# Kernel tuning notes

Hardware: AMD Instinct MI355X
Metric: run time of the kernel (lower is better)

The kernel has to match this reference:

```python
import jax, jax.numpy as jnp
import numpy as np
from jax import lax

B = 1024          # batch
R = 100           # number of radical heads (TOP_RADICALS)


def _conv(x, w, b, padding):
    y = lax.conv_general_dilated(
        x, w, window_strides=(1, 1), padding=padding,
        dimension_numbers=('NCHW', 'OIHW', 'NCHW'))
    return y + b[None, :, None, None]


def _maxpool2(x):
    return lax.reduce_window(x, -jnp.inf, lax.max,
                             (1, 1, 2, 2), (1, 1, 2, 2), 'VALID')


def setup_inputs() -> dict:
    key = jax.random.key(0)
    ks = jax.random.split(key, 20)
    s = 0.05
    inp = {
        'x': jax.random.normal(ks[0], (B, 1, 98, 98), jnp.float32),
        'conv1_w': jax.random.normal(ks[1], (6, 1, 3, 3), jnp.float32) * s,
        'conv1_b': jnp.zeros((6,), jnp.float32),
        'conv2_w': jax.random.normal(ks[2], (4, 6, 6, 6), jnp.float32) * s,
        'conv2_b': jnp.zeros((4,), jnp.float32),
        'conv3_w': jax.random.normal(ks[3], (2, 4, 3, 3), jnp.float32) * s,
        'conv3_b': jnp.zeros((2,), jnp.float32),
        'fc1_w': jax.random.normal(ks[4], (200, 400), jnp.float32) * s,
        'fc1_b': jnp.zeros((400,), jnp.float32),
        'fc2_w': jax.random.normal(ks[5], (400, 200), jnp.float32) * s,
        'fc2_b': jnp.zeros((200,), jnp.float32),
        # all R per-radical heads stacked: Linear(200,140)->(140,84)->(84,42)->(42,4)
        'h1_w': jax.random.normal(ks[6], (R, 200, 140), jnp.float32) * s,
        'h1_b': jnp.zeros((R, 140), jnp.float32),
        'h2_w': jax.random.normal(ks[7], (R, 140, 84), jnp.float32) * s,
        'h2_b': jnp.zeros((R, 84), jnp.float32),
        'h3_w': jax.random.normal(ks[8], (R, 84, 42), jnp.float32) * s,
        'h3_b': jnp.zeros((R, 42), jnp.float32),
        'h4_w': jax.random.normal(ks[9], (R, 42, 4), jnp.float32) * s,
        'h4_b': jnp.zeros((R, 4), jnp.float32),
    }
    return inp


def reference(x, conv1_w, conv1_b, conv2_w, conv2_b, conv3_w, conv3_b,
              fc1_w, fc1_b, fc2_w, fc2_b,
              h1_w, h1_b, h2_w, h2_b, h3_w, h3_b, h4_w, h4_b):
    # conv trunk: conv -> relu -> maxpool, x3
    x = _maxpool2(jax.nn.relu(_conv(x, conv1_w, conv1_b, [(1, 1), (1, 1)])))  # [B,6,49,49]
    x = _maxpool2(jax.nn.relu(_conv(x, conv2_w, conv2_b, 'VALID')))           # [B,4,22,22]
    x = _maxpool2(jax.nn.relu(_conv(x, conv3_w, conv3_b, 'VALID')))           # [B,2,10,10]
    x = x.reshape(x.shape[0], -1)                                             # [B,200]
    # shared MLP trunk
    x = jax.nn.relu(x @ fc1_w + fc1_b)   # [B,400]
    x = jax.nn.relu(x @ fc2_w + fc2_b)   # [B,200]
    # R independent 4-layer heads, fused into batched einsums
    h = jax.nn.relu(jnp.einsum('bd,rdh->brh', x, h1_w) + h1_b)  # [B,R,140]
    h = jax.nn.relu(jnp.einsum('brd,rdh->brh', h, h2_w) + h2_b)  # [B,R,84]
    h = jax.nn.relu(jnp.einsum('brd,rdh->brh', h, h3_w) + h3_b)  # [B,R,42]
    h = jnp.einsum('brd,rdh->brh', h, h4_w) + h4_b               # [B,R,4]
    # torch.cat over heads along dim=1 == reshape [B, R*4]
    return h.reshape(h.shape[0], -1)
```

## Files before the change

### kernel.cpp

```cpp
#include <hip/hip_runtime.h>

#define NB 1024
#define NR 100

typedef _Float16 half_t;
typedef half_t f16x8 __attribute__((ext_vector_type(8)));
typedef float f32x4 __attribute__((ext_vector_type(4)));

__device__ __forceinline__ int kmap2(int g, int j) {
    return g*4 + (j & 3) + ((j >> 2) << 4);
}

#define GLDS(gsrc, ldst) \
    __builtin_amdgcn_global_load_lds( \
        (const __attribute__((address_space(1))) void*)(gsrc), \
        (__attribute__((address_space(3))) void*)(ldst), 16, 0, 0)

__global__ __launch_bounds__(256) void conv1_k(const float* __restrict__ x,
        const float* __restrict__ w, const float* __restrict__ bias,
        float* __restrict__ out) {
    __shared__ float img[98*98];
    __shared__ float ws[54];
    __shared__ float bs[6];
    const int b = blockIdx.x;
    const int tid = threadIdx.x;
    const float* xb = x + (size_t)b * 9604;
    for (int i = tid; i < 2401; i += 256)
        ((float4*)img)[i] = ((const float4*)xb)[i];
    if (tid < 54) ws[tid] = w[tid];
    if (tid < 6) bs[tid] = bias[tid];
    __syncthreads();
    for (int pos = tid; pos < 2401; pos += 256) {
        const int py = pos / 49, px = pos % 49;
        const int y0 = 2*py - 1, x0 = 2*px - 1;
        float p[4][4];
        #pragma unroll
        for (int dy = 0; dy < 4; ++dy) {
            const int iy = y0 + dy;
            #pragma unroll
            for (int dx = 0; dx < 4; ++dx) {
                const int ix = x0 + dx;
                p[dy][dx] = (iy >= 0 && iy < 98 && ix >= 0 && ix < 98)
                            ? img[iy*98 + ix] : 0.f;
            }
        }
        #pragma unroll
        for (int c = 0; c < 6; ++c) {
            float v0 = bs[c], v1 = bs[c], v2 = bs[c], v3 = bs[c];
            #pragma unroll
            for (int ky = 0; ky < 3; ++ky) {
                #pragma unroll
                for (int kx = 0; kx < 3; ++kx) {
                    const float wv = ws[c*9 + ky*3 + kx];
                    v0 = fmaf(wv, p[ky  ][kx  ], v0);
                    v1 = fmaf(wv, p[ky  ][kx+1], v1);
                    v2 = fmaf(wv, p[ky+1][kx  ], v2);
                    v3 = fmaf(wv, p[ky+1][kx+1], v3);
                }
            }
            float m = fmaxf(fmaxf(v0, v1), fmaxf(v2, v3));
            out[((size_t)b*6 + c)*2401 + pos] = fmaxf(m, 0.f);
        }
    }
}

__global__ __launch_bounds__(256, 4) void conv2_k(const float* __restrict__ in,
        const float* __restrict__ w, const float* __restrict__ bias,
        float* __restrict__ out) {
    __shared__ float smc[6*27*28];
    __shared__ float ws[864];
    __shared__ float bs[4];
    const int blk = blockIdx.x;
    const int b  = blk >> 2;
    const int qy = (blk >> 1) & 1, qx = blk & 1;
    const int r0 = qy*22, c0 = qx*22;
    const int tid = threadIdx.x;
    const float* src = in + (size_t)b * 14406;
    for (int idx = tid; idx < 6*27*27; idx += 256) {
        const int ic  = idx / 729;
        const int rem = idx - ic*729;
        const int rr  = rem / 27;
        const int cc  = rem - rr*27;
        smc[ic*756 + rr*28 + cc] = src[ic*2401 + (r0+rr)*49 + c0 + cc];
    }
    for (int i = tid; i < 864; i += 256) ws[i] = w[i];
    if (tid < 4) bs[tid] = bias[tid];
    __syncthreads();
    if (tid < 242) {
        const int ocg = tid / 121;
        const int p   = tid - ocg*121;
        const int py  = p / 11, px = p - py*11;
        const int y0  = 2*py, x0 = 2*px;
        float acc[2][4];
        #pragma unroll
        for (int o = 0; o < 2; ++o) {
            const float bv = bs[ocg*2 + o];
            acc[o][0] = acc[o][1] = acc[o][2] = acc[o][3] = bv;
        }
        #pragma unroll
        for (int ic = 0; ic < 6; ++ic) {
            float pt[7][7];
            const float* basep = smc + ic*756 + y0*28 + x0;
            #pragma unroll
            for (int u = 0; u < 7; ++u) {
                const float* rb = basep + u*28;
                *(float2*)&pt[u][0] = *(const float2*)&rb[0];
                *(float2*)&pt[u][2] = *(const float2*)&rb[2];
                *(float2*)&pt[u][4] = *(const float2*)&rb[4];
                pt[u][6] = rb[6];
            }
            #pragma unroll
            for (int o = 0; o < 2; ++o) {
                const float* wp = ws + ((ocg*2 + o)*6 + ic)*36;
                #pragma unroll
                for (int ky = 0; ky < 6; ++ky) {
                    #pragma unroll
                    for (int kx = 0; kx < 6; ++kx) {
                        const float wv = wp[ky*6 + kx];
                        acc[o][0] = fmaf(wv, pt[ky  ][kx  ], acc[o][0]);
                        acc[o][1] = fmaf(wv, pt[ky  ][kx+1], acc[o][1]);
                        acc[o][2] = fmaf(wv, pt[ky+1][kx  ], acc[o][2]);
                        acc[o][3] = fmaf(wv, pt[ky+1][kx+1], acc[o][3]);
                    }
                }
            }
        }
        const int PY = qy*11 + py, PX = qx*11 + px;
        #pragma unroll
        for (int o = 0; o < 2; ++o) {
            const int oc = ocg*2 + o;
            float m = fmaxf(fmaxf(acc[o][0], acc[o][1]),
                            fmaxf(acc[o][2], acc[o][3]));
            out[(((size_t)b*4 + oc)*22 + PY)*22 + PX] = fmaxf(m, 0.f);
        }
    }
}

__global__ __launch_bounds__(256) void conv3_k(const float* __restrict__ in,
        const float* __restrict__ w, const float* __restrict__ bias,
        float* __restrict__ out) {
    __shared__ float sm[1936];
    __shared__ float ws[72];
    __shared__ float bs[2];
    const int b = blockIdx.x;
    const int tid = threadIdx.x;
    const float* src = in + (size_t)b * 1936;
    for (int i = tid; i < 484; i += 256)
        ((float4*)sm)[i] = ((const float4*)src)[i];
    if (tid < 72) ws[tid] = w[tid];
    if (tid < 2) bs[tid] = bias[tid];
    __syncthreads();
    if (tid < 200) {
        const int c = tid / 100;
        const int rem = tid % 100;
        const int py = rem / 10, px = rem % 10;
        const int y0 = 2*py, x0 = 2*px;
        float a0, a1, a2, a3;
        a0 = a1 = a2 = a3 = bs[c];
        #pragma unroll
        for (int ic = 0; ic < 4; ++ic) {
            float p[4][4];
            const float* base = sm + ic*484 + y0*22 + x0;
            #pragma unroll
            for (int u = 0; u < 4; ++u)
                #pragma unroll
                for (int v = 0; v < 4; ++v)
                    p[u][v] = base[u*22 + v];
            const float* wp = ws + (c*4 + ic)*9;
            #pragma unroll
            for (int ky = 0; ky < 3; ++ky) {
                #pragma unroll
                for (int kx = 0; kx < 3; ++kx) {
                    const float wv = wp[ky*3 + kx];
                    a0 = fmaf(wv, p[ky  ][kx  ], a0);
                    a1 = fmaf(wv, p[ky  ][kx+1], a1);
                    a2 = fmaf(wv, p[ky+1][kx  ], a2);
                    a3 = fmaf(wv, p[ky+1][kx+1], a3);
                }
            }
        }
        float m = fmaxf(fmaxf(a0, a1), fmaxf(a2, a3));
        out[(size_t)b*200 + tid] = fmaxf(m, 0.f);
    }
}

template<bool G0OUT>
__global__ __launch_bounds__(256, 4) void gemm_k(
        const float* __restrict__ A, int lda,
        const float* __restrict__ W, const float* __restrict__ bias,
        float* __restrict__ C, int ldc,
        int M, int N, int K,
        half_t* __restrict__ g0h, half_t* __restrict__ g0l) {
    __shared__ float As[32][132];
    __shared__ float Ws[32][64];
    const int m0 = blockIdx.y * 128;
    const int n0 = blockIdx.x * 64;
    const int tid = threadIdx.x;
    const int ti = tid >> 4, tj = tid & 15;
    float acc[8][4];
    #pragma unroll
    for (int i = 0; i < 8; ++i)
        #pragma unroll
        for (int j = 0; j < 4; ++j) acc[i][j] = 0.f;

    for (int k0 = 0; k0 < K; k0 += 32) {
        #pragma unroll
        for (int i = 0; i < 4; ++i) {
            const int f = tid + i*256;
            const int m = f >> 3, kg = f & 7;
            const int kk = kg*4;
            float4 v = make_float4(0.f, 0.f, 0.f, 0.f);
            if (k0 + kk < K)
                v = *(const float4*)(A + (long)(m0 + m)*lda + k0 + kk);
            As[kk+0][m] = v.x;
            As[kk+1][m] = v.y;
            As[kk+2][m] = v.z;
            As[kk+3][m] = v.w;
        }
        #pragma unroll
        for (int i = 0; i < 2; ++i) {
            const int f = tid + i*256;
            const int kk = f >> 4, cg = f & 15;
            const int n = n0 + cg*4;
            float4 v = make_float4(0.f, 0.f, 0.f, 0.f);
            if (k0 + kk < K) {
                const float* wp = W + (long)(k0 + kk)*N;
                if (n + 3 < N) v = *(const float4*)(wp + n);
                else {
                    if (n+0 < N) v.x = wp[n+0];
                    if (n+1 < N) v.y = wp[n+1];
                    if (n+2 < N) v.z = wp[n+2];
                }
            }
            *(float4*)&Ws[kk][cg*4] = v;
        }
        __syncthreads();
        #pragma unroll
        for (int kk = 0; kk < 32; ++kk) {
            float a[8], wv[4];
            *(float4*)&a[0] = *(const float4*)&As[kk][ti*8];
            *(float4*)&a[4] = *(const float4*)&As[kk][ti*8 + 4];
            *(float4*)&wv[0] = *(const float4*)&Ws[kk][tj*4];
            #pragma unroll
            for (int i = 0; i < 8; ++i)
                #pragma unroll
                for (int j = 0; j < 4; ++j)
                    acc[i][j] = fmaf(a[i], wv[j], acc[i][j]);
        }
        __syncthreads();
    }

    const int nb = n0 + tj*4;
    float bv[4] = {0.f, 0.f, 0.f, 0.f};
    #pragma unroll
    for (int e = 0; e < 4; ++e) if (nb + e < N) bv[e] = bias[nb + e];

    if (!G0OUT) {
        #pragma unroll
        for (int i = 0; i < 8; ++i) {
            const long m = m0 + ti*8 + i;
            if (nb + 3 < N) {
                float4 v;
                v.x = fmaxf(acc[i][0] + bv[0], 0.f);
                v.y = fmaxf(acc[i][1] + bv[1], 0.f);
                v.z = fmaxf(acc[i][2] + bv[2], 0.f);
                v.w = fmaxf(acc[i][3] + bv[3], 0.f);
                *(float4*)(C + m*(long)ldc + nb) = v;
            } else {
                #pragma unroll
                for (int j = 0; j < 4; ++j)
                    if (nb + j < N)
                        C[m*(long)ldc + nb + j] = fmaxf(acc[i][j] + bv[j], 0.f);
            }
        }
    } else {
        #pragma unroll
        for (int i = 0; i < 8; ++i) {
            const int m = m0 + ti*8 + i;
            #pragma unroll
            for (int j = 0; j < 4; ++j) {
                const int k = nb + j;
                if (k < N) {
                    const float v = fmaxf(acc[i][j] + bv[j], 0.f);
                    const half_t hi = (half_t)v;
                    const half_t lo = (half_t)(v - (float)hi);
                    const int kc = k >> 5, klo = k & 31;
                    const int h = klo >> 4, rm = klo & 15;
                    const int gg = rm >> 2, rr = rm & 3;
                    const size_t idx =
                        ((size_t)((m >> 4)*7 + kc)*64 + (gg << 4) + (m & 15))*8
                        + h*4 + rr;
                    g0h[idx] = hi;
                    g0l[idx] = lo;
                }
            }
        }
    }
}

__global__ __launch_bounds__(256) void wsplit_k(
        const float* __restrict__ w1, const float* __restrict__ w2,
        const float* __restrict__ w3, const float* __restrict__ w4,
        half_t* __restrict__ f1h, half_t* __restrict__ f1l,
        half_t* __restrict__ f2h, half_t* __restrict__ f2l,
        half_t* __restrict__ f3h, half_t* __restrict__ f3l,
        half_t* __restrict__ f4h, half_t* __restrict__ f4l) {
    __shared__ float lds[32*140];
    const int cx = blockIdx.x, r = blockIdx.y, tid = threadIdx.x;
    int K, N, KC, NF, kc;
    const float* src;
    half_t *dh, *dl;
    if (cx < 7)       { K=200; N=140; KC=7; NF=9; kc=cx;    src=w1; dh=f1h; dl=f1l; }
    else if (cx < 12) { K=140; N=84;  KC=5; NF=6; kc=cx-7;  src=w2; dh=f2h; dl=f2l; }
    else if (cx < 15) { K=84;  N=42;  KC=3; NF=3; kc=cx-12; src=w3; dh=f3h; dl=f3l; }
    else              { K=42;  N=4;   KC=2; NF=1; kc=cx-15; src=w4; dh=f4h; dl=f4l; }
    const float* sb = src + (size_t)r * K * N;
    for (int i = tid; i < 32*N; i += 256) {
        const int kk = i / N, n = i - kk*N;
        const int kg = kc*32 + kk;
        lds[kk*N + n] = (kg < K) ? sb[(size_t)kg*N + n] : 0.f;
    }
    __syncthreads();
    const size_t base = ((size_t)r*KC + kc)*NF*512;
    for (int e = tid; e < NF*512; e += 256) {
        const int nf = e >> 9, rem = e & 511;
        const int l = rem >> 3, j = rem & 7;
        const int g = l >> 4, c = l & 15;
        const int kl = kmap2(g, j);
        const int n = nf*16 + c;
        const float v = (n < N) ? lds[kl*N + n] : 0.f;
        const half_t hi = (half_t)v;
        const half_t lo = (half_t)(v - (float)hi);
        dh[base + (size_t)nf*512 + rem] = hi;
        dl[base + (size_t)nf*512 + rem] = lo;
    }
}

#define MFMA(a, b, c) __builtin_amdgcn_mfma_f32_16x16x32_f16(a, b, c, 0, 0, 0)

__global__ __launch_bounds__(256, 4) void head_k(
        const half_t* __restrict__ g0h, const half_t* __restrict__ g0l,
        const half_t* __restrict__ w1h, const half_t* __restrict__ w1l,
        const half_t* __restrict__ w2h, const half_t* __restrict__ w2l,
        const half_t* __restrict__ w3h, const half_t* __restrict__ w3l,
        const half_t* __restrict__ w4h, const half_t* __restrict__ w4l,
        const float* __restrict__ b1, const float* __restrict__ b2,
        const float* __restrict__ b3, const float* __restrict__ b4,
        float* __restrict__ out) {
    __shared__ half_t wb[18*512];
    __shared__ float bl[270];
    const int bid = blockIdx.x;
    const int cx  = bid & 7;
    const int kb  = bid >> 3;
    const int r   = ((kb >> 3) << 3) + cx;
    if (r >= NR) return;
    const int mt  = kb & 7;
    const int tid = threadIdx.x;
    if (tid < 140) bl[tid]       = b1[(size_t)r*140 + tid];
    if (tid < 84)  bl[140 + tid] = b2[(size_t)r*84  + tid];
    if (tid < 42)  bl[224 + tid] = b3[(size_t)r*42  + tid];
    if (tid < 4)   bl[266 + tid] = b4[(size_t)r*4   + tid];
    const int w = tid >> 6, l = tid & 63;
    const int g4 = ((l >> 4) & 3) * 4;
    const int mb0 = mt*8 + w*2;
    const size_t loff = (size_t)l * 8;

    f32x4 a1[2][9] = {};
    for (int kc = 0; kc < 7; ++kc) {
        const half_t* hs = w1h + ((size_t)r*7 + kc)*9*512;
        const half_t* ls = w1l + ((size_t)r*7 + kc)*9*512;
        #pragma unroll
        for (int p0 = 0; p0 < 3; ++p0) {
            const int p = w + p0*4;
            if (p < 9) {
                GLDS(hs + (size_t)p*512 + loff, wb + p*512);
                GLDS(ls + (size_t)p*512 + loff, wb + (9+p)*512);
            }
        }
        f16x8 bh[2], blo[2];
        #pragma unroll
        for (int mb = 0; mb < 2; ++mb) {
            const size_t bo = ((size_t)(mb0 + mb)*7 + kc)*512 + loff;
            bh[mb]  = *(const f16x8*)(g0h + bo);
            blo[mb] = *(const f16x8*)(g0l + bo);
        }
        __syncthreads();
        #pragma unroll
        for (int nf = 0; nf < 9; ++nf) {
            const f16x8 wh = *(const f16x8*)(wb + nf*512 + loff);
            const f16x8 wl = *(const f16x8*)(wb + (9+nf)*512 + loff);
            #pragma unroll
            for (int mb = 0; mb < 2; ++mb) {
                a1[mb][nf] = MFMA(wh, bh[mb],  a1[mb][nf]);
                a1[mb][nf] = MFMA(wh, blo[mb], a1[mb][nf]);
                a1[mb][nf] = MFMA(wl, bh[mb],  a1[mb][nf]);
            }
        }
        __syncthreads();
    }
    f16x8 b2h[2][5], b2l[2][5];
    #pragma unroll
    for (int kc = 0; kc < 5; ++kc)
        #pragma unroll
        for (int h = 0; h < 2; ++h) {
            const int nf = kc*2 + h;
            #pragma unroll
            for (int mb = 0; mb < 2; ++mb)
                #pragma unroll
                for (int rr = 0; rr < 4; ++rr) {
                    float v = 0.f;
                    if (nf < 9) {
                        const int n = nf*16 + g4 + rr;
                        v = (n < 140) ? fmaxf(a1[mb][nf][rr] + bl[n], 0.f) : 0.f;
                    }
                    const half_t hi = (half_t)v;
                    const half_t lo = (half_t)(v - (float)hi);
                    b2h[mb][kc][h*4+rr] = hi;
                    b2l[mb][kc][h*4+rr] = lo;
                }
        }
    f32x4 a2[2][6] = {};
    for (int kc = 0; kc < 5; ++kc) {
        const half_t* hs = w2h + ((size_t)r*5 + kc)*6*512;
        const half_t* ls = w2l + ((size_t)r*5 + kc)*6*512;
        #pragma unroll
        for (int p0 = 0; p0 < 2; ++p0) {
            const int p = w + p0*4;
            if (p < 6) {
                GLDS(hs + (size_t)p*512 + loff, wb + p*512);
                GLDS(ls + (size_t)p*512 + loff, wb + (6+p)*512);
            }
        }
        __syncthreads();
        #pragma unroll
        for (int nf = 0; nf < 6; ++nf) {
            const f16x8 wh = *(const f16x8*)(wb + nf*512 + loff);
            const f16x8 wl = *(const f16x8*)(wb + (6+nf)*512 + loff);
            #pragma unroll
            for (int mb = 0; mb < 2; ++mb) {
                a2[mb][nf] = MFMA(wh, b2h[mb][kc], a2[mb][nf]);
                a2[mb][nf] = MFMA(wh, b2l[mb][kc], a2[mb][nf]);
                a2[mb][nf] = MFMA(wl, b2h[mb][kc], a2[mb][nf]);
            }
        }
        __syncthreads();
    }
    f16x8 b3h[2][3], b3l[2][3];
    #pragma unroll
    for (int kc = 0; kc < 3; ++kc)
        #pragma unroll
        for (int h = 0; h < 2; ++h) {
            const int nf = kc*2 + h;
            #pragma unroll
            for (int mb = 0; mb < 2; ++mb)
                #pragma unroll
                for (int rr = 0; rr < 4; ++rr) {
                    float v = 0.f;
                    if (nf < 6) {
                        const int n = nf*16 + g4 + rr;
                        v = (n < 84) ? fmaxf(a2[mb][nf][rr] + bl[140 + n], 0.f) : 0.f;
                    }
                    const half_t hi = (half_t)v;
                    const half_t lo = (half_t)(v - (float)hi);
                    b3h[mb][kc][h*4+rr] = hi;
                    b3l[mb][kc][h*4+rr] = lo;
                }
        }
    f32x4 a3[2][3] = {};
    for (int kc = 0; kc < 3; ++kc) {
        const half_t* hs = w3h + ((size_t)r*3 + kc)*3*512;
        const half_t* ls = w3l + ((size_t)r*3 + kc)*3*512;
        {
            const int p = w;
            if (p < 3) {
                GLDS(hs + (size_t)p*512 + loff, wb + p*512);
                GLDS(ls + (size_t)p*512 + loff, wb + (3+p)*512);
            }
        }
        __syncthreads();
        #pragma unroll
        for (int nf = 0; nf < 3; ++nf) {
            const f16x8 wh = *(const f16x8*)(wb + nf*512 + loff);
            const f16x8 wl = *(const f16x8*)(wb + (3+nf)*512 + loff);
            #pragma unroll
            for (int mb = 0; mb < 2; ++mb) {
                a3[mb][nf] = MFMA(wh, b3h[mb][kc], a3[mb][nf]);
                a3[mb][nf] = MFMA(wh, b3l[mb][kc], a3[mb][nf]);
                a3[mb][nf] = MFMA(wl, b3h[mb][kc], a3[mb][nf]);
            }
        }
        __syncthreads();
    }
    f16x8 b4h[2][2], b4l[2][2];
    #pragma unroll
    for (int kc = 0; kc < 2; ++kc)
        #pragma unroll
        for (int h = 0; h < 2; ++h) {
            const int nf = kc*2 + h;
            #pragma unroll
            for (int mb = 0; mb < 2; ++mb)
                #pragma unroll
                for (int rr = 0; rr < 4; ++rr) {
                    float v = 0.f;
                    if (nf < 3) {
                        const int n = nf*16 + g4 + rr;
                        v = (n < 42) ? fmaxf(a3[mb][nf][rr] + bl[224 + n], 0.f) : 0.f;
                    }
                    const half_t hi = (half_t)v;
                    const half_t lo = (half_t)(v - (float)hi);
                    b4h[mb][kc][h*4+rr] = hi;
                    b4l[mb][kc][h*4+rr] = lo;
                }
        }
    f32x4 a4[2] = {};
    #pragma unroll
    for (int kc = 0; kc < 2; ++kc) {
        const size_t wo = ((size_t)r*2 + kc)*512 + loff;
        const f16x8 wh = *(const f16x8*)(w4h + wo);
        const f16x8 wl = *(const f16x8*)(w4l + wo);
        #pragma unroll
        for (int mb = 0; mb < 2; ++mb) {
            a4[mb] = MFMA(wh, b4h[mb][kc], a4[mb]);
            a4[mb] = MFMA(wh, b4l[mb][kc], a4[mb]);
            a4[mb] = MFMA(wl, b4h[mb][kc], a4[mb]);
        }
    }
    if ((l >> 4) == 0) {
        #pragma unroll
        for (int mb = 0; mb < 2; ++mb) {
            const int b = (mb0 + mb)*16 + (l & 15);
            float4 o;
            o.x = a4[mb][0] + bl[266];
            o.y = a4[mb][1] + bl[267];
            o.z = a4[mb][2] + bl[268];
            o.w = a4[mb][3] + bl[269];
            *(float4*)(out + (size_t)b*400 + r*4) = o;
        }
    }
}

extern "C" void kernel_launch(void* const* d_in, const int* in_sizes, int n_in,
                              void* d_out, int out_size, void* d_ws, size_t ws_size,
                              hipStream_t stream) {
    const float* x    = (const float*)d_in[0];
    const float* c1w  = (const float*)d_in[1];
    const float* c1b  = (const float*)d_in[2];
    const float* c2w  = (const float*)d_in[3];
    const float* c2b  = (const float*)d_in[4];
    const float* c3w  = (const float*)d_in[5];
    const float* c3b  = (const float*)d_in[6];
    const float* fc1w = (const float*)d_in[7];
    const float* fc1b = (const float*)d_in[8];
    const float* fc2w = (const float*)d_in[9];
    const float* fc2b = (const float*)d_in[10];
    const float* h1w  = (const float*)d_in[11];
    const float* h1b  = (const float*)d_in[12];
    const float* h2w  = (const float*)d_in[13];
    const float* h2b  = (const float*)d_in[14];
    const float* h3w  = (const float*)d_in[15];
    const float* h3b  = (const float*)d_in[16];
    const float* h4w  = (const float*)d_in[17];
    const float* h4b  = (const float*)d_in[18];
    float* out = (float*)d_out;

    char* ws = (char*)d_ws;
    size_t o = 0;
    float* t1 = (float*)(ws + o); o += (size_t)NB*6*2401*4;
    float* t2 = (float*)(ws + o); o += (size_t)NB*4*484*4;
    float* t3 = (float*)(ws + o); o += (size_t)NB*200*4;
    float* f1 = (float*)(ws + o); o += (size_t)NB*400*4;
    half_t* g0h = (half_t*)(ws + o); o += (size_t)64*7*512*2;
    half_t* g0l = (half_t*)(ws + o); o += (size_t)64*7*512*2;
    half_t* w1h = (half_t*)(ws + o); o += (size_t)NR*7*9*512*2;
    half_t* w1l = (half_t*)(ws + o); o += (size_t)NR*7*9*512*2;
    half_t* w2h = (half_t*)(ws + o); o += (size_t)NR*5*6*512*2;
    half_t* w2l = (half_t*)(ws + o); o += (size_t)NR*5*6*512*2;
    half_t* w3h = (half_t*)(ws + o); o += (size_t)NR*3*3*512*2;
    half_t* w3l = (half_t*)(ws + o); o += (size_t)NR*3*3*512*2;
    half_t* w4h = (half_t*)(ws + o); o += (size_t)NR*2*1*512*2;
    half_t* w4l = (half_t*)(ws + o); o += (size_t)NR*2*1*512*2;

    hipMemsetAsync(g0h, 0, (size_t)64*7*512*2*2, stream);

    wsplit_k<<<dim3(17, NR), 256, 0, stream>>>(h1w, h2w, h3w, h4w,
        w1h, w1l, w2h, w2l, w3h, w3l, w4h, w4l);

    conv1_k<<<NB, 256, 0, stream>>>(x, c1w, c1b, t1);
    conv2_k<<<NB*4, 256, 0, stream>>>(t1, c2w, c2b, t2);
    conv3_k<<<NB, 256, 0, stream>>>(t2, c3w, c3b, t3);

    gemm_k<false><<<dim3(7, 8), 256, 0, stream>>>(
        t3, 200, fc1w, fc1b, f1, 400, NB, 400, 200, nullptr, nullptr);
    gemm_k<true><<<dim3(4, 8), 256, 0, stream>>>(
        f1, 400, fc2w, fc2b, nullptr, 0, NB, 200, 400, g0h, g0l);

    head_k<<<832, 256, 0, stream>>>(
        g0h, g0l, w1h, w1l, w2h, w2l, w3h, w3l, w4h, w4l,
        h1b, h2b, h3b, h4b, out);

    (void)in_sizes; (void)n_in; (void)out_size; (void)ws_size;
}
```

Baseline: 220.8 us.

## Restructure conv2 to compute 2x4 outputs per thread with swizzled LDS rows

conv2 now splits each image into two half-height blocks instead of four quadrants. Each thread computes two output channels over a 2x4 pre-pool window, giving two pooled outputs, and reuses each loaded input row across kernel rows. The input tile is staged in LDS with 64-float rows and an XOR swizzle meant to avoid bank conflicts. Weights and biases in all three conv kernels are read directly from global memory as wave-uniform scalar loads instead of being staged in LDS. This raises register pressure and halves the block count, but cuts LDS traffic and per-output load overhead.

After: 244.7 us. 10.8% more time.

```diff
diff --git a/kernel.cpp b/kernel.cpp
--- a/kernel.cpp
+++ b/kernel.cpp
@@ -20,15 +20,11 @@
         const float* __restrict__ w, const float* __restrict__ bias,
         float* __restrict__ out) {
     __shared__ float img[98*98];
-    __shared__ float ws[54];
-    __shared__ float bs[6];
     const int b = blockIdx.x;
     const int tid = threadIdx.x;
     const float* xb = x + (size_t)b * 9604;
     for (int i = tid; i < 2401; i += 256)
         ((float4*)img)[i] = ((const float4*)xb)[i];
-    if (tid < 54) ws[tid] = w[tid];
-    if (tid < 6) bs[tid] = bias[tid];
     __syncthreads();
     for (int pos = tid; pos < 2401; pos += 256) {
         const int py = pos / 49, px = pos % 49;
@@ -46,12 +42,13 @@
         }
         #pragma unroll
         for (int c = 0; c < 6; ++c) {
-            float v0 = bs[c], v1 = bs[c], v2 = bs[c], v3 = bs[c];
+            const float bv = bias[c];
+            float v0 = bv, v1 = bv, v2 = bv, v3 = bv;
             #pragma unroll
             for (int ky = 0; ky < 3; ++ky) {
                 #pragma unroll
                 for (int kx = 0; kx < 3; ++kx) {
-                    const float wv = ws[c*9 + ky*3 + kx];
+                    const float wv = w[c*9 + ky*3 + kx];
                     v0 = fmaf(wv, p[ky  ][kx  ], v0);
                     v1 = fmaf(wv, p[ky  ][kx+1], v1);
                     v2 = fmaf(wv, p[ky+1][kx  ], v2);
@@ -64,75 +61,92 @@
     }
 }
 
+#define SWZ(r, c) ((c) ^ ((((r) >> 1) & 3) << 3))
+
 __global__ __launch_bounds__(256, 4) void conv2_k(const float* __restrict__ in,
         const float* __restrict__ w, const float* __restrict__ bias,
         float* __restrict__ out) {
-    __shared__ float smc[6*27*28];
-    __shared__ float ws[864];
-    __shared__ float bs[4];
+    __shared__ float smc[6*27*64];
     const int blk = blockIdx.x;
-    const int b  = blk >> 2;
-    const int qy = (blk >> 1) & 1, qx = blk & 1;
-    const int r0 = qy*22, c0 = qx*22;
+    const int b  = blk >> 1;
+    const int qb = blk & 1;
+    const int r0 = qb * 22;
     const int tid = threadIdx.x;
     const float* src = in + (size_t)b * 14406;
-    for (int idx = tid; idx < 6*27*27; idx += 256) {
-        const int ic  = idx / 729;
-        const int rem = idx - ic*729;
-        const int rr  = rem / 27;
-        const int cc  = rem - rr*27;
-        smc[ic*756 + rr*28 + cc] = src[ic*2401 + (r0+rr)*49 + c0 + cc];
-    }
-    for (int i = tid; i < 864; i += 256) ws[i] = w[i];
-    if (tid < 4) bs[tid] = bias[tid];
+    for (int ic = 0; ic < 6; ++ic)
+        for (int j = tid; j < 1323; j += 256) {
+            const int rr = j / 49, cc = j - rr*49;
+            smc[ic*1728 + rr*64 + SWZ(rr, cc)] =
+                src[ic*2401 + (size_t)(r0 + rr)*49 + cc];
+        }
     __syncthreads();
-    if (tid < 242) {
-        const int ocg = tid / 121;
-        const int p   = tid - ocg*121;
-        const int py  = p / 11, px = p - py*11;
-        const int y0  = 2*py, x0 = 2*px;
-        float acc[2][4];
-        #pragma unroll
-        for (int o = 0; o < 2; ++o) {
-            const float bv = bs[ocg*2 + o];
-            acc[o][0] = acc[o][1] = acc[o][2] = acc[o][3] = bv;
-        }
-        #pragma unroll
-        for (int ic = 0; ic < 6; ++ic) {
-            float pt[7][7];
-            const float* basep = smc + ic*756 + y0*28 + x0;
-            #pragma unroll
-            for (int u = 0; u < 7; ++u) {
-                const float* rb = basep + u*28;
-                *(float2*)&pt[u][0] = *(const float2*)&rb[0];
-                *(float2*)&pt[u][2] = *(const float2*)&rb[2];
-                *(float2*)&pt[u][4] = *(const float2*)&rb[4];
-                pt[u][6] = rb[6];
-            }
-            #pragma unroll
-            for (int o = 0; o < 2; ++o) {
-                const float* wp = ws + ((ocg*2 + o)*6 + ic)*36;
-                #pragma unroll
-                for (int ky = 0; ky < 6; ++ky) {
+
+    const int wv_ = tid >> 6;
+    const int ocg = __builtin_amdgcn_readfirstlane(tid >> 7);
+    const int unit = ((wv_ & 1) << 6) | (tid & 63);
+    if (unit >= 121) return;
+    const int py = unit / 11, q = unit - py*11;
+    const int y0 = 2*py;
+    const int x0 = 4*q;
+
+    int aofs[7][5];
+    #pragma unroll
+    for (int u = 0; u < 7; ++u) {
+        const int rr = y0 + u;
+        #pragma unroll
+        for (int vi = 0; vi < 5; ++vi)
+            aofs[u][vi] = (rr*64 + SWZ(rr, x0 + 2*vi)) * 4;
+    }
+
+    const float* wg = w + (size_t)ocg * 432;
+    float acc[2][2][4];
+    #pragma unroll
+    for (int o = 0; o < 2; ++o) {
+        const float bv = bias[ocg*2 + o];
+        #pragma unroll
+        for (int dy = 0; dy < 2; ++dy)
+            #pragma unroll
+            for (int dx = 0; dx < 4; ++dx) acc[o][dy][dx] = bv;
+    }
+
+    #pragma unroll
+    for (int ic = 0; ic < 6; ++ic) {
+        const char* plane = (const char*)smc + ic*6912;
+        #pragma unroll
+        for (int u = 0; u < 7; ++u) {
+            float pr[9];
+            #pragma unroll
+            for (int vi = 0; vi < 4; ++vi)
+                *(float2*)&pr[vi*2] = *(const float2*)(plane + aofs[u][vi]);
+            pr[8] = *(const float*)(plane + aofs[u][4]);
+            #pragma unroll
+            for (int dy = 0; dy < 2; ++dy) {
+                const int ky = u - dy;
+                if (ky < 0 || ky > 5) continue;
+                #pragma unroll
+                for (int kx = 0; kx < 6; ++kx) {
+                    const float w0 = wg[      ic*36 + ky*6 + kx];
+                    const float w1 = wg[216 + ic*36 + ky*6 + kx];
                     #pragma unroll
-                    for (int kx = 0; kx < 6; ++kx) {
-                        const float wv = wp[ky*6 + kx];
-                        acc[o][0] = fmaf(wv, pt[ky  ][kx  ], acc[o][0]);
-                        acc[o][1] = fmaf(wv, pt[ky  ][kx+1], acc[o][1]);
-                        acc[o][2] = fmaf(wv, pt[ky+1][kx  ], acc[o][2]);
-                        acc[o][3] = fmaf(wv, pt[ky+1][kx+1], acc[o][3]);
+                    for (int dx = 0; dx < 4; ++dx) {
+                        acc[0][dy][dx] = fmaf(w0, pr[dx+kx], acc[0][dy][dx]);
+                        acc[1][dy][dx] = fmaf(w1, pr[dx+kx], acc[1][dy][dx]);
                     }
                 }
             }
         }
-        const int PY = qy*11 + py, PX = qx*11 + px;
-        #pragma unroll
-        for (int o = 0; o < 2; ++o) {
-            const int oc = ocg*2 + o;
-            float m = fmaxf(fmaxf(acc[o][0], acc[o][1]),
-                            fmaxf(acc[o][2], acc[o][3]));
-            out[(((size_t)b*4 + oc)*22 + PY)*22 + PX] = fmaxf(m, 0.f);
-        }
+    }
+
+    const int PY = qb*11 + py;
+    #pragma unroll
+    for (int o = 0; o < 2; ++o) {
+        const int oc = ocg*2 + o;
+        float2 ov;
+        ov.x = fmaxf(fmaxf(fmaxf(acc[o][0][0], acc[o][0][1]),
+                           fmaxf(acc[o][1][0], acc[o][1][1])), 0.f);
+        ov.y = fmaxf(fmaxf(fmaxf(acc[o][0][2], acc[o][0][3]),
+                           fmaxf(acc[o][1][2], acc[o][1][3])), 0.f);
+        *(float2*)(out + (((size_t)b*4 + oc)*22 + PY)*22 + 2*q) = ov;
     }
 }
 
@@ -140,15 +154,11 @@
         const float* __restrict__ w, const float* __restrict__ bias,
         float* __restrict__ out) {
     __shared__ float sm[1936];
-    __shared__ float ws[72];
-    __shared__ float bs[2];
     const int b = blockIdx.x;
     const int tid = threadIdx.x;
     const float* src = in + (size_t)b * 1936;
     for (int i = tid; i < 484; i += 256)
         ((float4*)sm)[i] = ((const float4*)src)[i];
-    if (tid < 72) ws[tid] = w[tid];
-    if (tid < 2) bs[tid] = bias[tid];
     __syncthreads();
     if (tid < 200) {
         const int c = tid / 100;
@@ -156,7 +166,7 @@
         const int py = rem / 10, px = rem % 10;
         const int y0 = 2*py, x0 = 2*px;
         float a0, a1, a2, a3;
-        a0 = a1 = a2 = a3 = bs[c];
+        a0 = a1 = a2 = a3 = bias[c];
         #pragma unroll
         for (int ic = 0; ic < 4; ++ic) {
             float p[4][4];
@@ -166,12 +176,11 @@
                 #pragma unroll
                 for (int v = 0; v < 4; ++v)
                     p[u][v] = base[u*22 + v];
-            const float* wp = ws + (c*4 + ic)*9;
             #pragma unroll
             for (int ky = 0; ky < 3; ++ky) {
                 #pragma unroll
                 for (int kx = 0; kx < 3; ++kx) {
-                    const float wv = wp[ky*3 + kx];
+                    const float wv = w[(c*4 + ic)*9 + ky*3 + kx];
                     a0 = fmaf(wv, p[ky  ][kx  ], a0);
                     a1 = fmaf(wv, p[ky  ][kx+1], a1);
                     a2 = fmaf(wv, p[ky+1][kx  ], a2);
@@ -586,7 +595,7 @@
         w1h, w1l, w2h, w2l, w3h, w3l, w4h, w4l);
 
     conv1_k<<<NB, 256, 0, stream>>>(x, c1w, c1b, t1);
-    conv2_k<<<NB*4, 256, 0, stream>>>(t1, c2w, c2b, t2);
+    conv2_k<<<NB*2, 256, 0, stream>>>(t1, c2w, c2b, t2);
     conv3_k<<<NB, 256, 0, stream>>>(t2, c3w, c3b, t3);
 
     gemm_k<false><<<dim3(7, 8), 256, 0, stream>>>(
```
